# Kernel tuning notes

Measured on AMD Instinct MI355X. Metric: run time of the kernel, lower is better.

Reference implementation:

```python
import jax, jax.numpy as jnp
import numpy as np

N_NODES = 50000
N_EDGES = 800000
IN_DIM = 16
HID = 128
OUT_DIM = 1
N_LAYERS = 2


def setup_inputs() -> dict:
    key = jax.random.key(0)
    ks = jax.random.split(key, 16)
    s = 0.05
    inp = {
        "edge_feats": jax.random.normal(ks[0], (N_EDGES, IN_DIM), jnp.float32),
        "node_feats": jax.random.normal(ks[1], (N_NODES, 4), jnp.float32),
        "src": jax.random.randint(ks[2], (N_EDGES,), 0, N_NODES, jnp.int32),
        "dst": jax.random.randint(ks[3], (N_EDGES,), 0, N_NODES, jnp.int32),
        # edge_embedding (dead in original forward, kept for faithfulness)
        "W_eemb": jax.random.normal(ks[4], (IN_DIM, HID), jnp.float32) * s,
        "b_eemb": jnp.zeros((HID,), jnp.float32),
        # node_embedding: Linear(4, hidden)
        "W_nemb": jax.random.normal(ks[5], (4, HID), jnp.float32) * s,
        "b_nemb": jnp.zeros((HID,), jnp.float32),
        # stacked GraphConv weights [n_layers, H, H]
        "gnn_W": jax.random.normal(ks[6], (N_LAYERS, HID, HID), jnp.float32) * s,
        "gnn_b": jnp.zeros((N_LAYERS, HID), jnp.float32),
        # output MLP
        "out_W1": jax.random.normal(ks[7], (HID, HID), jnp.float32) * s,
        "out_b1": jnp.zeros((HID,), jnp.float32),
        "out_W2": jax.random.normal(ks[8], (HID, OUT_DIM), jnp.float32) * s,
        "out_b2": jnp.zeros((OUT_DIM,), jnp.float32),
    }
    return inp


def reference(edge_feats, node_feats, src, dst, W_eemb, b_eemb, W_nemb, b_nemb,
              gnn_W, gnn_b, out_W1, out_b1, out_W2, out_b2):
    ones = jnp.ones((src.shape[0],), jnp.float32)
    deg_out = jnp.clip(jax.ops.segment_sum(ones, src, num_segments=N_NODES), 1.0)
    deg_in = jnp.clip(jax.ops.segment_sum(ones, dst, num_segments=N_NODES), 1.0)
    norm_out = deg_out ** -0.5  # [N]
    norm_in = deg_in ** -0.5    # [N]

    # edge_embedding output is dead code in the original forward (overwritten)
    _h_e = edge_feats @ W_eemb + b_eemb

    h = node_feats @ W_nemb + b_nemb  # [N, H]
    for l in range(N_LAYERS):
        # DGL GraphConv norm='both': D_out^{-1/2} gather -> scatter-sum -> D_in^{-1/2} -> W, b
        hs = h * norm_out[:, None]
        agg = jax.ops.segment_sum(hs[src], dst, num_segments=N_NODES)  # [N, H]
        h = agg * norm_in[:, None]
        h = h @ gnn_W[l] + gnn_b[l]
        h = jax.nn.relu(h)

    edge_h = h[src] + h[dst]  # apply_edges UDF, [E, H]
    x = jax.nn.relu(edge_h @ out_W1 + out_b1)
    return x @ out_W2 + out_b2  # [E, OUT_DIM]
```

## Files before the change

kernel.cpp:

```cpp
#include <hip/hip_runtime.h>

#define N_NODES 50000
#define N_EDGES 800000
#define HID 128
#define NB 256
#define NPB 196
#define TP 136

typedef __attribute__((ext_vector_type(8))) short bf16x8;
typedef __attribute__((ext_vector_type(4))) float f32x4;

__device__ __forceinline__ unsigned pack2bf(float a, float b) {
  unsigned ua = __float_as_uint(a);
  ua += 0x7FFFu + ((ua >> 16) & 1u);
  unsigned ub = __float_as_uint(b);
  ub += 0x7FFFu + ((ub >> 16) & 1u);
  return (ua >> 16) | (ub & 0xFFFF0000u);
}
#define BFLO(u) __uint_as_float((u) << 16)
#define BFHI(u) __uint_as_float((u) & 0xFFFF0000u)

__device__ __forceinline__ float2 unpk(unsigned u) {
  return make_float2(BFLO(u), BFHI(u));
}
__device__ __forceinline__ float2 f2add(float2 a, float2 b) {
  return make_float2(a.x + b.x, a.y + b.y);
}
__device__ __forceinline__ float2 f2max0(float2 a) {
  return make_float2(fmaxf(a.x, 0.f), fmaxf(a.y, 0.f));
}
__device__ __forceinline__ float2 f2fma(float2 a, float2 b, float2 c) {
  return make_float2(fmaf(a.x, b.x, c.x), fmaf(a.y, b.y, c.y));
}


__global__ __launch_bounds__(256) void p1_hist_kernel(
    const int* __restrict__ src, const int* __restrict__ dst,
    int* __restrict__ bcnt_d, int* __restrict__ bcnt_s) {
  __shared__ int hd[NB], hs[NB];
  int t = threadIdx.x;
  hd[t] = 0; hs[t] = 0;
  __syncthreads();
  for (int e = blockIdx.x * 256 + t; e < N_EDGES; e += gridDim.x * 256) {
    atomicAdd(&hd[dst[e] / NPB], 1);
    atomicAdd(&hs[src[e] / NPB], 1);
  }
  __syncthreads();
  if (hd[t]) atomicAdd(&bcnt_d[t], hd[t]);
  if (hs[t]) atomicAdd(&bcnt_s[t], hs[t]);
}

__global__ void p2_scan_kernel(const int* __restrict__ bcnt_d, const int* __restrict__ bcnt_s,
                               int* __restrict__ bofs_d, int* __restrict__ bofs_s,
                               int* __restrict__ cur_d, int* __restrict__ cur_s) {
  __shared__ int s[NB];
  int t = threadIdx.x;
  int v = bcnt_d[t];
  s[t] = v;
  __syncthreads();
  for (int o = 1; o < NB; o <<= 1) {
    int x = (t >= o) ? s[t - o] : 0;
    __syncthreads();
    s[t] += x;
    __syncthreads();
  }
  int ofs = s[t] - v;
  bofs_d[t] = ofs; cur_d[t] = ofs;
  if (t == NB - 1) bofs_d[NB] = s[t];
  __syncthreads();
  v = bcnt_s[t];
  s[t] = v;
  __syncthreads();
  for (int o = 1; o < NB; o <<= 1) {
    int x = (t >= o) ? s[t - o] : 0;
    __syncthreads();
    s[t] += x;
    __syncthreads();
  }
  ofs = s[t] - v;
  bofs_s[t] = ofs; cur_s[t] = ofs;
  if (t == NB - 1) bofs_s[NB] = s[t];
}

__global__ __launch_bounds__(256) void p3_scatter_both_kernel(
    const int* __restrict__ src, const int* __restrict__ dst,
    int* __restrict__ cur_d, int* __restrict__ cur_s,
    int2* __restrict__ sdst, int* __restrict__ ssrc) {
  __shared__ int bcd[NB], bbd[NB], bcs[NB], bbs[NB];
  int t = threadIdx.x;
  int base = blockIdx.x * 2048;
  bcd[t] = 0; bcs[t] = 0;
  __syncthreads();
  int mybd[8], myrd[8], mys[8], myp[8], mybs[8], myrs[8];
#pragma unroll
  for (int u = 0; u < 8; ++u) {
    int e = base + u * 256 + t;
    mybd[u] = -1;
    if (e < N_EDGES) {
      int s = src[e], d = dst[e];
      int bd = d / NPB;
      mybd[u] = bd;
      myrd[u] = atomicAdd(&bcd[bd], 1);
      mys[u] = s;
      myp[u] = ((d - bd * NPB) << 20) | e;
      int bs = s / NPB;
      mybs[u] = bs;
      myrs[u] = atomicAdd(&bcs[bs], 1);
    }
  }
  __syncthreads();
  {
    int cd = bcd[t];
    if (cd) bbd[t] = atomicAdd(&cur_d[t], cd);
    int cs = bcs[t];
    if (cs) bbs[t] = atomicAdd(&cur_s[t], cs);
  }
  __syncthreads();
#pragma unroll
  for (int u = 0; u < 8; ++u) {
    if (mybd[u] >= 0) {
      sdst[bbd[mybd[u]] + myrd[u]] = make_int2(mys[u], myp[u]);
      ssrc[bbs[mybs[u]] + myrs[u]] = mys[u];
    }
  }
}

__global__ __launch_bounds__(256) void p4_csr_kernel(
    const int2* __restrict__ sdst, const int* __restrict__ bofs_d,
    int* __restrict__ row_ofs, float* __restrict__ norm_in,
    int* __restrict__ csr_src, int* __restrict__ csr_eid) {
  __shared__ int hc[NB], sc[NB], cur[NB];
  int b = blockIdx.x, t = threadIdx.x;
  int base = bofs_d[b], cnt = bofs_d[b + 1] - base;
  hc[t] = 0;
  __syncthreads();
  for (int i = t; i < cnt; i += 256) atomicAdd(&hc[sdst[base + i].y >> 20], 1);
  __syncthreads();
  int v = hc[t];
  sc[t] = v;
  __syncthreads();
  for (int o = 1; o < NB; o <<= 1) {
    int x = (t >= o) ? sc[t - o] : 0;
    __syncthreads();
    sc[t] += x;
    __syncthreads();
  }
  int ofs = sc[t] - v;
  int node = b * NPB + t;
  if (t < NPB && node < N_NODES) {
    row_ofs[node] = base + ofs;
    norm_in[node] = rsqrtf((float)(v < 1 ? 1 : v));
  }
  cur[t] = base + ofs;
  if (b == 0 && t == 0) row_ofs[N_NODES] = N_EDGES;
  __syncthreads();
  for (int i = t; i < cnt; i += 256) {
    int2 e = sdst[base + i];
    int pos = atomicAdd(&cur[e.y >> 20], 1);
    csr_src[pos] = e.x;
    csr_eid[pos] = e.y & 0xFFFFF;
  }
}

__global__ __launch_bounds__(256) void p5_degout_kernel(
    const int* __restrict__ ssrc, const int* __restrict__ bofs_s,
    float* __restrict__ norm_out) {
  __shared__ int hc[NB];
  int b = blockIdx.x, t = threadIdx.x;
  int base = bofs_s[b], cnt = bofs_s[b + 1] - base;
  int lo = b * NPB;
  hc[t] = 0;
  __syncthreads();
  for (int i = t; i < cnt; i += 256) atomicAdd(&hc[ssrc[base + i] - lo], 1);
  __syncthreads();
  int node = lo + t;
  if (t < NPB && node < N_NODES) {
    int v = hc[t];
    norm_out[node] = rsqrtf((float)(v < 1 ? 1 : v));
  }
}

__global__ __launch_bounds__(256) void prep_w_kernel(
    const float* __restrict__ Wa, const float* __restrict__ Wb,
    const float* __restrict__ Wc, short* __restrict__ Wta,
    short* __restrict__ Wtb, short* __restrict__ Wtc) {
  int t = blockIdx.x * 256 + threadIdx.x;
  if (t < HID * HID) {
    int k = t >> 7, n = t & 127;
    Wta[n * HID + k] = (short)(pack2bf(Wa[t], 0.f) & 0xFFFFu);
    Wtb[n * HID + k] = (short)(pack2bf(Wb[t], 0.f) & 0xFFFFu);
    Wtc[n * HID + k] = (short)(pack2bf(Wc[t], 0.f) & 0xFFFFu);
  }
}


__global__ __launch_bounds__(256) void agg4_kernel(
    const float4* __restrict__ nf4, const float* __restrict__ no_,
    const int* __restrict__ csr_src, const int* __restrict__ row_ofs,
    float4* __restrict__ agg4, float* __restrict__ sno) {
  int wid = (blockIdx.x * blockDim.x + threadIdx.x) >> 6;
  int lane = threadIdx.x & 63;
  int g = lane >> 4, l = lane & 15;
  int v = wid * 4 + g;
  if (v >= N_NODES) return;
  int beg = row_ofs[v], end = row_ofs[v + 1];
  float ax = 0.f, ay = 0.f, az = 0.f, aw = 0.f, sn = 0.f;
  for (int i = beg + l; i < end; i += 16) {
    int s = csr_src[i];
    float w = no_[s];
    float4 n = nf4[s];
    ax += n.x * w; ay += n.y * w; az += n.z * w; aw += n.w * w;
    sn += w;
  }
#pragma unroll
  for (int o = 1; o < 16; o <<= 1) {
    ax += __shfl_xor(ax, o, 16);
    ay += __shfl_xor(ay, o, 16);
    az += __shfl_xor(az, o, 16);
    aw += __shfl_xor(aw, o, 16);
    sn += __shfl_xor(sn, o, 16);
  }
  if (l == 0) {
    agg4[v] = make_float4(ax, ay, az, aw);
    sno[v] = sn;
  }
}

__global__ __launch_bounds__(256) void gemm_l1_mfma(
    const float4* __restrict__ agg4, const float* __restrict__ sno,
    const float* __restrict__ ni_, const float* __restrict__ no_,
    const float* __restrict__ Wn, const float* __restrict__ bn,
    const short* __restrict__ Wt0, const float* __restrict__ b0,
    short* __restrict__ h1b, int nrows) {
  int t = threadIdx.x;
  int w = t >> 6, lane = t & 63;
  int m16 = lane & 15, quad = lane >> 4;
  int v0 = blockIdx.x * 64;
  int row = v0 + w * 16 + m16;
  bool rvalid = row < nrows;
  int rc = rvalid ? row : (nrows - 1);
  float4 a = agg4[rc];
  float sn = sno[rc], nin = ni_[rc];

  bf16x8 xfr[4];
#pragma unroll
  for (int kc = 0; kc < 4; ++kc) {
    union { unsigned u[4]; bf16x8 v; } cv;
#pragma unroll
    for (int jj = 0; jj < 4; ++jj) {
      int k0 = kc * 32 + quad * 8 + jj * 2;
      float x0 = (a.x * Wn[k0] + a.y * Wn[HID + k0] + a.z * Wn[2 * HID + k0] +
                  a.w * Wn[3 * HID + k0] + bn[k0] * sn) * nin;
      int k1 = k0 + 1;
      float x1 = (a.x * Wn[k1] + a.y * Wn[HID + k1] + a.z * Wn[2 * HID + k1] +
                  a.w * Wn[3 * HID + k1] + bn[k1] * sn) * nin;
      cv.u[jj] = pack2bf(x0, x1);
    }
    xfr[kc] = cv.v;
  }
  f32x4 acc[8];
#pragma unroll
  for (int nt = 0; nt < 8; ++nt) {
    acc[nt][0] = 0.f; acc[nt][1] = 0.f; acc[nt][2] = 0.f; acc[nt][3] = 0.f;
  }
#pragma unroll
  for (int nt = 0; nt < 8; ++nt) {
    const bf16x8* Wr = (const bf16x8*)(Wt0 + (size_t)(nt * 16 + m16) * HID);
#pragma unroll
    for (int kc = 0; kc < 4; ++kc)
      acc[nt] = __builtin_amdgcn_mfma_f32_16x16x32_bf16(Wr[kc * 4 + quad], xfr[kc],
                                                        acc[nt], 0, 0, 0);
  }
  if (rvalid) {
    float nov = no_[row];
#pragma unroll
    for (int nt = 0; nt < 8; ++nt) {
      int nb = nt * 16 + quad * 4;
      float4 bv = *(const float4*)&b0[nb];
      float r0 = fmaxf(acc[nt][0] + bv.x, 0.f) * nov;
      float r1 = fmaxf(acc[nt][1] + bv.y, 0.f) * nov;
      float r2 = fmaxf(acc[nt][2] + bv.z, 0.f) * nov;
      float r3 = fmaxf(acc[nt][3] + bv.w, 0.f) * nov;
      uint2 pk;
      pk.x = pack2bf(r0, r1);
      pk.y = pack2bf(r2, r3);
      *(uint2*)(h1b + (size_t)row * HID + nb) = pk;
    }
  }
}

__global__ __launch_bounds__(256) void aggregate_kernel(
    const uint4* __restrict__ hb, const int* __restrict__ row_ofs,
    const int* __restrict__ csr_src, const float* __restrict__ ni_,
    uint4* __restrict__ Ab) {
  int v = (blockIdx.x * blockDim.x + threadIdx.x) >> 6;
  int lane = threadIdx.x & 63;
  if (v >= N_NODES) return;
  int beg = row_ofs[v], end = row_ofs[v + 1];
  int g = lane >> 4, l = lane & 15;
  float2 acc2[4];
#pragma unroll
  for (int j = 0; j < 4; ++j) acc2[j] = make_float2(0.f, 0.f);
  for (int i = beg; i < end; i += 16) {
    int ss[4];
#pragma unroll
    for (int u = 0; u < 4; ++u) {
      int ii = i + 4 * u + g;
      ss[u] = (ii < end) ? csr_src[ii] : N_NODES;
    }
    uint4 X[4];
#pragma unroll
    for (int u = 0; u < 4; ++u) X[u] = hb[(size_t)ss[u] * 16 + l];
#pragma unroll
    for (int u = 0; u < 4; ++u) {
      acc2[0] = f2add(acc2[0], unpk(X[u].x));
      acc2[1] = f2add(acc2[1], unpk(X[u].y));
      acc2[2] = f2add(acc2[2], unpk(X[u].z));
      acc2[3] = f2add(acc2[3], unpk(X[u].w));
    }
  }
#pragma unroll
  for (int j = 0; j < 4; ++j) {
    acc2[j].x += __shfl_xor(acc2[j].x, 16, 64);
    acc2[j].x += __shfl_xor(acc2[j].x, 32, 64);
    acc2[j].y += __shfl_xor(acc2[j].y, 16, 64);
    acc2[j].y += __shfl_xor(acc2[j].y, 32, 64);
  }
  if (g == 0) {
    float n = ni_[v];
    uint4 pk;
    pk.x = pack2bf(acc2[0].x * n, acc2[0].y * n);
    pk.y = pack2bf(acc2[1].x * n, acc2[1].y * n);
    pk.z = pack2bf(acc2[2].x * n, acc2[2].y * n);
    pk.w = pack2bf(acc2[3].x * n, acc2[3].y * n);
    Ab[(size_t)v * 16 + l] = pk;
  }
}

__global__ __launch_bounds__(256) void gemm_dual_mfma(
    const short* __restrict__ Ab, const short* __restrict__ Wt0,
    const float* __restrict__ b0, const short* __restrict__ Wt1,
    short* __restrict__ yb, int nrows) {
  __shared__ short T1s[4][16 * TP];
  int t = threadIdx.x;
  int w = t >> 6, lane = t & 63;
  int m16 = lane & 15, quad = lane >> 4;
  int v0 = blockIdx.x * 64;
  int row = v0 + w * 16 + m16;
  bool rvalid = row < nrows;
  int rc = rvalid ? row : (nrows - 1);

  bf16x8 xfr[4];
  {
    const bf16x8* Ar = (const bf16x8*)(Ab + (size_t)rc * HID);
#pragma unroll
    for (int kc = 0; kc < 4; ++kc) xfr[kc] = Ar[kc * 4 + quad];
  }
  f32x4 acc[8];
#pragma unroll
  for (int nt = 0; nt < 8; ++nt) {
    acc[nt][0] = 0.f; acc[nt][1] = 0.f; acc[nt][2] = 0.f; acc[nt][3] = 0.f;
  }
#pragma unroll
  for (int nt = 0; nt < 8; ++nt) {
    const bf16x8* Wr = (const bf16x8*)(Wt0 + (size_t)(nt * 16 + m16) * HID);
#pragma unroll
    for (int kc = 0; kc < 4; ++kc)
      acc[nt] = __builtin_amdgcn_mfma_f32_16x16x32_bf16(Wr[kc * 4 + quad], xfr[kc],
                                                        acc[nt], 0, 0, 0);
  }
  short* T1w = &T1s[w][0];
#pragma unroll
  for (int nt = 0; nt < 8; ++nt) {
    int nb = nt * 16 + quad * 4;
    float4 bv = *(const float4*)&b0[nb];
    float r0 = fmaxf(acc[nt][0] + bv.x, 0.f);
    float r1 = fmaxf(acc[nt][1] + bv.y, 0.f);
    float r2 = fmaxf(acc[nt][2] + bv.z, 0.f);
    float r3 = fmaxf(acc[nt][3] + bv.w, 0.f);
    uint2 pk;
    pk.x = pack2bf(r0, r1);
    pk.y = pack2bf(r2, r3);
    *(uint2*)&T1w[m16 * TP + nb] = pk;
    acc[nt][0] = 0.f; acc[nt][1] = 0.f; acc[nt][2] = 0.f; acc[nt][3] = 0.f;
  }
  __syncthreads();
  bf16x8 tfr[4];
#pragma unroll
  for (int kc = 0; kc < 4; ++kc)
    tfr[kc] = *(const bf16x8*)&T1w[m16 * TP + kc * 32 + quad * 8];
#pragma unroll
  for (int nt = 0; nt < 8; ++nt) {
    const bf16x8* Wr = (const bf16x8*)(Wt1 + (size_t)(nt * 16 + m16) * HID);
#pragma unroll
    for (int kc = 0; kc < 4; ++kc)
      acc[nt] = __builtin_amdgcn_mfma_f32_16x16x32_bf16(Wr[kc * 4 + quad], tfr[kc],
                                                        acc[nt], 0, 0, 0);
  }
  if (rvalid) {
#pragma unroll
    for (int nt = 0; nt < 8; ++nt) {
      int nb = nt * 16 + quad * 4;
      uint2 pk;
      pk.x = pack2bf(acc[nt][0], acc[nt][1]);
      pk.y = pack2bf(acc[nt][2], acc[nt][3]);
      *(uint2*)(yb + (size_t)row * HID + nb) = pk;
    }
  }
}

__global__ __launch_bounds__(256) void edge_out_kernel(
    const int* __restrict__ csr_src, const int* __restrict__ csr_eid,
    const int* __restrict__ row_ofs, const uint4* __restrict__ yb,
    const float* __restrict__ b1, const float* __restrict__ w2,
    const float* __restrict__ b2, float* __restrict__ out) {
  int v = (blockIdx.x * blockDim.x + threadIdx.x) >> 6;
  int lane = threadIdx.x & 63;
  if (v >= N_NODES) return;
  int beg = row_ofs[v], end = row_ofs[v + 1];
  if (beg >= end) return;
  int g = lane >> 4, l = lane & 15;
  const float2* b12 = (const float2*)b1;
  const float2* w22 = (const float2*)w2;
  uint4 D = yb[(size_t)v * 16 + l];
  float2 d0 = f2add(unpk(D.x), b12[l * 4 + 0]);
  float2 d1 = f2add(unpk(D.y), b12[l * 4 + 1]);
  float2 d2 = f2add(unpk(D.z), b12[l * 4 + 2]);
  float2 d3 = f2add(unpk(D.w), b12[l * 4 + 3]);
  float2 w0 = w22[l * 4 + 0], w1 = w22[l * 4 + 1];
  float2 w2v = w22[l * 4 + 2], w3 = w22[l * 4 + 3];
  float ob2 = b2[0];
  for (int i = beg; i < end; i += 16) {
    int ii[4]; bool qq[4]; int ss[4];
#pragma unroll
    for (int u = 0; u < 4; ++u) {
      ii[u] = i + 4 * u + g;
      qq[u] = ii[u] < end;
      ss[u] = csr_src[qq[u] ? ii[u] : beg];
    }
    uint4 A[4];
#pragma unroll
    for (int u = 0; u < 4; ++u) A[u] = yb[(size_t)ss[u] * 16 + l];
#pragma unroll
    for (int u = 0; u < 4; ++u) {
      float2 p2;
      p2.x = 0.f; p2.y = 0.f;
      p2 = f2fma(f2max0(f2add(unpk(A[u].x), d0)), w0, p2);
      p2 = f2fma(f2max0(f2add(unpk(A[u].y), d1)), w1, p2);
      p2 = f2fma(f2max0(f2add(unpk(A[u].z), d2)), w2v, p2);
      p2 = f2fma(f2max0(f2add(unpk(A[u].w), d3)), w3, p2);
      float p = p2.x + p2.y;
      p += __shfl_down(p, 8, 16);
      p += __shfl_down(p, 4, 16);
      p += __shfl_down(p, 2, 16);
      p += __shfl_down(p, 1, 16);
      if (l == 0 && qq[u]) out[csr_eid[ii[u]]] = p + ob2;
    }
  }
}

extern "C" void kernel_launch(void* const* d_in, const int* in_sizes, int n_in,
                              void* d_out, int out_size, void* d_ws, size_t ws_size,
                              hipStream_t stream) {
  const float* node_feats = (const float*)d_in[1];
  const int*   src        = (const int*)d_in[2];
  const int*   dst        = (const int*)d_in[3];
  const float* W_nemb     = (const float*)d_in[6];
  const float* b_nemb     = (const float*)d_in[7];
  const float* gnn_W      = (const float*)d_in[8];
  const float* gnn_b      = (const float*)d_in[9];
  const float* out_W1     = (const float*)d_in[10];
  const float* out_b1     = (const float*)d_in[11];
  const float* out_W2     = (const float*)d_in[12];
  const float* out_b2     = (const float*)d_in[13];
  float* out = (float*)d_out;

  size_t off = 0;
  char* base = (char*)d_ws;
  auto alloc = [&](size_t nbytes) -> char* {
    off = (off + 255) & ~(size_t)255;
    char* p = base + off;
    off += nbytes;
    return p;
  };
  int*    bcnt2    = (int*)alloc(2 * NB * 4);
  int*    bofs_d   = (int*)alloc((NB + 1) * 4);
  int*    bofs_s   = (int*)alloc((NB + 1) * 4);
  int*    cur_d    = (int*)alloc(NB * 4);
  int*    cur_s    = (int*)alloc(NB * 4);
  float*  norm_out = (float*)alloc(N_NODES * 4);
  float*  norm_in  = (float*)alloc(N_NODES * 4);
  int*    row_ofs  = (int*)alloc((N_NODES + 1) * 4);
  int*    csr_src  = (int*)alloc((size_t)N_EDGES * 4);
  int*    csr_eid  = (int*)alloc((size_t)N_EDGES * 4);
  float4* agg4     = (float4*)alloc((size_t)N_NODES * 16);
  float*  sno      = (float*)alloc(N_NODES * 4);
  short*  Wta      = (short*)alloc((size_t)HID * HID * 2);
  short*  Wtb      = (short*)alloc((size_t)HID * HID * 2);
  short*  Wtc     = (short*)alloc((size_t)HID * HID * 2);
  short*  h1b      = (short*)alloc((size_t)(N_NODES + 1) * HID * 2);
  short*  Ab       = (short*)alloc((size_t)N_NODES * HID * 2);
  short*  ybs      = (short*)alloc((size_t)N_NODES * HID * 2);
  int2*   sdst     = (int2*)Ab;
  int*    ssrc     = (int*)ybs;
  int*    bcnt_d   = bcnt2;
  int*    bcnt_s   = bcnt2 + NB;
  (void)ws_size; (void)n_in; (void)in_sizes; (void)out_size;

  hipMemsetAsync(bcnt2, 0, 2 * NB * 4, stream);
  hipMemsetAsync(h1b + (size_t)N_NODES * HID, 0, HID * 2, stream);
  prep_w_kernel<<<(HID * HID + 255) / 256, 256, 0, stream>>>(
      gnn_W, gnn_W + (size_t)HID * HID, out_W1, Wta, Wtb, Wtc);
  p1_hist_kernel<<<128, 256, 0, stream>>>(src, dst, bcnt_d, bcnt_s);
  p2_scan_kernel<<<1, 256, 0, stream>>>(bcnt_d, bcnt_s, bofs_d, bofs_s, cur_d, cur_s);
  p3_scatter_both_kernel<<<(N_EDGES + 2047) / 2048, 256, 0, stream>>>(
      src, dst, cur_d, cur_s, sdst, ssrc);
  p4_csr_kernel<<<NB, 256, 0, stream>>>(sdst, bofs_d, row_ofs, norm_in, csr_src, csr_eid);
  p5_degout_kernel<<<NB, 256, 0, stream>>>(ssrc, bofs_s, norm_out);

  agg4_kernel<<<(N_NODES * 16 + 255) / 256, 256, 0, stream>>>(
      (const float4*)node_feats, norm_out, csr_src, row_ofs, agg4, sno);
  gemm_l1_mfma<<<(N_NODES + 63) / 64, 256, 0, stream>>>(
      agg4, sno, norm_in, norm_out, W_nemb, b_nemb, Wta, gnn_b, h1b, N_NODES);

  aggregate_kernel<<<(N_NODES * 64 + 255) / 256, 256, 0, stream>>>(
      (const uint4*)h1b, row_ofs, csr_src, norm_in, (uint4*)Ab);

  gemm_dual_mfma<<<(N_NODES + 63) / 64, 256, 0, stream>>>(
      Ab, Wtb, gnn_b + HID, Wtc, ybs, N_NODES);

  edge_out_kernel<<<(N_NODES * 64 + 255) / 256, 256, 0, stream>>>(
      csr_src, csr_eid, row_ofs, (const uint4*)ybs, out_b1, out_W2, out_b2, out);
}
```

Measured before the change: 309.5 us.

## Switch to fp16 storage and MFMA, fuse prep kernels, rewrite edge output per-edge

Replaces bf16 with fp16 throughout: fp16 MFMA, packed conversions via cvt_pkrtz, and the edge dot product done with packed half adds and fdot2. The weight-prep work is folded into the scan kernel and the degree-out pass into the CSR kernel, which cuts the number of launches. The edge output kernel now uses one thread per edge with a new csr_dst array, and half of out_b1 is folded into each node's y so the edge sum carries the full bias. In exchange fp16 has less range than bf16, each thread loads 512 bytes per edge with no reuse across lanes, and the extra csr_dst array costs memory traffic.

```diff
diff --git a/kernel.cpp b/kernel.cpp
--- a/kernel.cpp
+++ b/kernel.cpp
@@ -7,30 +7,44 @@
 #define NPB 196
 #define TP 136
 
-typedef __attribute__((ext_vector_type(8))) short bf16x8;
+typedef __attribute__((ext_vector_type(8))) _Float16 f16x8;
+typedef __attribute__((ext_vector_type(2))) _Float16 h2v;
+typedef __attribute__((ext_vector_type(2))) __fp16 fp16v2;
 typedef __attribute__((ext_vector_type(4))) float f32x4;
-
-__device__ __forceinline__ unsigned pack2bf(float a, float b) {
-  unsigned ua = __float_as_uint(a);
-  ua += 0x7FFFu + ((ua >> 16) & 1u);
-  unsigned ub = __float_as_uint(b);
-  ub += 0x7FFFu + ((ub >> 16) & 1u);
-  return (ua >> 16) | (ub & 0xFFFF0000u);
-}
-#define BFLO(u) __uint_as_float((u) << 16)
-#define BFHI(u) __uint_as_float((u) & 0xFFFF0000u)
-
-__device__ __forceinline__ float2 unpk(unsigned u) {
-  return make_float2(BFLO(u), BFHI(u));
-}
-__device__ __forceinline__ float2 f2add(float2 a, float2 b) {
-  return make_float2(a.x + b.x, a.y + b.y);
-}
-__device__ __forceinline__ float2 f2max0(float2 a) {
-  return make_float2(fmaxf(a.x, 0.f), fmaxf(a.y, 0.f));
-}
-__device__ __forceinline__ float2 f2fma(float2 a, float2 b, float2 c) {
-  return make_float2(fmaf(a.x, b.x, c.x), fmaf(a.y, b.y, c.y));
+typedef __attribute__((ext_vector_type(2))) float f32x2;
+
+__device__ __forceinline__ unsigned pkh(float a, float b) {
+  union { fp16v2 h; unsigned u; } c;
+  c.h = __builtin_amdgcn_cvt_pkrtz(a, b);
+  return c.u;
+}
+__device__ __forceinline__ h2v u2h(unsigned u) {
+  union { unsigned u; h2v h; } c;
+  c.u = u;
+  return c.h;
+}
+__device__ __forceinline__ f32x2 unpkh(unsigned u) {
+  h2v h = u2h(u);
+  f32x2 r;
+  r[0] = (float)h[0];
+  r[1] = (float)h[1];
+  return r;
+}
+__device__ __forceinline__ short f2hs(float f) {
+  union { _Float16 h; short s; } c;
+  c.h = (_Float16)f;
+  return c.s;
+}
+__device__ __forceinline__ float edot(unsigned a, unsigned b, unsigned w, float acc) {
+  h2v r = u2h(a) + u2h(b);
+  h2v z = {(_Float16)0.f, (_Float16)0.f};
+  r = __builtin_elementwise_max(r, z);
+#if __has_builtin(__builtin_amdgcn_fdot2)
+  return __builtin_amdgcn_fdot2(r, u2h(w), acc, false);
+#else
+  h2v wv = u2h(w);
+  return acc + (float)r[0] * (float)wv[0] + (float)r[1] * (float)wv[1];
+#endif
 }
 
 
@@ -50,9 +64,33 @@
   if (hs[t]) atomicAdd(&bcnt_s[t], hs[t]);
 }
 
-__global__ void p2_scan_kernel(const int* __restrict__ bcnt_d, const int* __restrict__ bcnt_s,
-                               int* __restrict__ bofs_d, int* __restrict__ bofs_s,
-                               int* __restrict__ cur_d, int* __restrict__ cur_s) {
+__global__ void p2_scan_prep_kernel(
+    const int* __restrict__ bcnt_d, const int* __restrict__ bcnt_s,
+    int* __restrict__ bofs_d, int* __restrict__ bofs_s,
+    int* __restrict__ cur_d, int* __restrict__ cur_s,
+    const float* __restrict__ Wa, const float* __restrict__ Wb,
+    const float* __restrict__ Wc, const float* __restrict__ w2f,
+    short* __restrict__ Wta, short* __restrict__ Wtb, short* __restrict__ Wtc,
+    unsigned* __restrict__ w2h, short* __restrict__ h1bz) {
+  int b = blockIdx.x;
+  if (b > 0) {
+    int t = (b - 1) * 256 + threadIdx.x;
+    if (t < HID * HID) {
+      int k = t >> 7, n = t & 127;
+      Wta[n * HID + k] = f2hs(Wa[t]);
+      Wtb[n * HID + k] = f2hs(Wb[t]);
+      Wtc[n * HID + k] = f2hs(Wc[t]);
+    }
+    if (b == 1) {
+      int t0 = threadIdx.x;
+      if (t0 < 64) {
+        w2h[t0] = pkh(w2f[2 * t0], w2f[2 * t0 + 1]);
+      } else if (t0 < 128) {
+        ((unsigned*)h1bz)[t0 - 64] = 0u;
+      }
+    }
+    return;
+  }
   __shared__ int s[NB];
   int t = threadIdx.x;
   int v = bcnt_d[t];
@@ -125,12 +163,30 @@
   }
 }
 
-__global__ __launch_bounds__(256) void p4_csr_kernel(
+__global__ __launch_bounds__(256) void p45_kernel(
     const int2* __restrict__ sdst, const int* __restrict__ bofs_d,
     int* __restrict__ row_ofs, float* __restrict__ norm_in,
-    int* __restrict__ csr_src, int* __restrict__ csr_eid) {
+    int* __restrict__ csr_src, int* __restrict__ csr_eid, int* __restrict__ csr_dst,
+    const int* __restrict__ ssrc, const int* __restrict__ bofs_s,
+    float* __restrict__ norm_out) {
   __shared__ int hc[NB], sc[NB], cur[NB];
-  int b = blockIdx.x, t = threadIdx.x;
+  int t = threadIdx.x;
+  if (blockIdx.x >= NB) {
+    int b = blockIdx.x - NB;
+    int base = bofs_s[b], cnt = bofs_s[b + 1] - base;
+    int lo = b * NPB;
+    hc[t] = 0;
+    __syncthreads();
+    for (int i = t; i < cnt; i += 256) atomicAdd(&hc[ssrc[base + i] - lo], 1);
+    __syncthreads();
+    int node = lo + t;
+    if (t < NPB && node < N_NODES) {
+      int v = hc[t];
+      norm_out[node] = rsqrtf((float)(v < 1 ? 1 : v));
+    }
+    return;
+  }
+  int b = blockIdx.x;
   int base = bofs_d[b], cnt = bofs_d[b + 1] - base;
   hc[t] = 0;
   __syncthreads();
@@ -156,40 +212,11 @@
   __syncthreads();
   for (int i = t; i < cnt; i += 256) {
     int2 e = sdst[base + i];
-    int pos = atomicAdd(&cur[e.y >> 20], 1);
+    int loc = e.y >> 20;
+    int pos = atomicAdd(&cur[loc], 1);
     csr_src[pos] = e.x;
     csr_eid[pos] = e.y & 0xFFFFF;
-  }
-}
-
-__global__ __launch_bounds__(256) void p5_degout_kernel(
-    const int* __restrict__ ssrc, const int* __restrict__ bofs_s,
-    float* __restrict__ norm_out) {
-  __shared__ int hc[NB];
-  int b = blockIdx.x, t = threadIdx.x;
-  int base = bofs_s[b], cnt = bofs_s[b + 1] - base;
-  int lo = b * NPB;
-  hc[t] = 0;
-  __syncthreads();
-  for (int i = t; i < cnt; i += 256) atomicAdd(&hc[ssrc[base + i] - lo], 1);
-  __syncthreads();
-  int node = lo + t;
-  if (t < NPB && node < N_NODES) {
-    int v = hc[t];
-    norm_out[node] = rsqrtf((float)(v < 1 ? 1 : v));
-  }
-}
-
-__global__ __launch_bounds__(256) void prep_w_kernel(
-    const float* __restrict__ Wa, const float* __restrict__ Wb,
-    const float* __restrict__ Wc, short* __restrict__ Wta,
-    short* __restrict__ Wtb, short* __restrict__ Wtc) {
-  int t = blockIdx.x * 256 + threadIdx.x;
-  if (t < HID * HID) {
-    int k = t >> 7, n = t & 127;
-    Wta[n * HID + k] = (short)(pack2bf(Wa[t], 0.f) & 0xFFFFu);
-    Wtb[n * HID + k] = (short)(pack2bf(Wb[t], 0.f) & 0xFFFFu);
-    Wtc[n * HID + k] = (short)(pack2bf(Wc[t], 0.f) & 0xFFFFu);
+    csr_dst[pos] = b * NPB + loc;
   }
 }
 
@@ -242,10 +269,10 @@
   float4 a = agg4[rc];
   float sn = sno[rc], nin = ni_[rc];
 
-  bf16x8 xfr[4];
+  f16x8 xfr[4];
 #pragma unroll
   for (int kc = 0; kc < 4; ++kc) {
-    union { unsigned u[4]; bf16x8 v; } cv;
+    union { unsigned u[4]; f16x8 v; } cv;
 #pragma unroll
     for (int jj = 0; jj < 4; ++jj) {
       int k0 = kc * 32 + quad * 8 + jj * 2;
@@ -254,7 +281,7 @@
       int k1 = k0 + 1;
       float x1 = (a.x * Wn[k1] + a.y * Wn[HID + k1] + a.z * Wn[2 * HID + k1] +
                   a.w * Wn[3 * HID + k1] + bn[k1] * sn) * nin;
-      cv.u[jj] = pack2bf(x0, x1);
+      cv.u[jj] = pkh(x0, x1);
     }
     xfr[kc] = cv.v;
   }
@@ -265,11 +292,11 @@
   }
 #pragma unroll
   for (int nt = 0; nt < 8; ++nt) {
-    const bf16x8* Wr = (const bf16x8*)(Wt0 + (size_t)(nt * 16 + m16) * HID);
+    const f16x8* Wr = (const f16x8*)(Wt0 + (size_t)(nt * 16 + m16) * HID);
 #pragma unroll
     for (int kc = 0; kc < 4; ++kc)
-      acc[nt] = __builtin_amdgcn_mfma_f32_16x16x32_bf16(Wr[kc * 4 + quad], xfr[kc],
-                                                        acc[nt], 0, 0, 0);
+      acc[nt] = __builtin_amdgcn_mfma_f32_16x16x32_f16(Wr[kc * 4 + quad], xfr[kc],
+                                                       acc[nt], 0, 0, 0);
   }
   if (rvalid) {
     float nov = no_[row];
@@ -282,8 +309,8 @@
       float r2 = fmaxf(acc[nt][2] + bv.z, 0.f) * nov;
       float r3 = fmaxf(acc[nt][3] + bv.w, 0.f) * nov;
       uint2 pk;
-      pk.x = pack2bf(r0, r1);
-      pk.y = pack2bf(r2, r3);
+      pk.x = pkh(r0, r1);
+      pk.y = pkh(r2, r3);
       *(uint2*)(h1b + (size_t)row * HID + nb) = pk;
     }
   }
@@ -298,9 +325,9 @@
   if (v >= N_NODES) return;
   int beg = row_ofs[v], end = row_ofs[v + 1];
   int g = lane >> 4, l = lane & 15;
-  float2 acc2[4];
-#pragma unroll
-  for (int j = 0; j < 4; ++j) acc2[j] = make_float2(0.f, 0.f);
+  f32x2 acc2[4];
+#pragma unroll
+  for (int j = 0; j < 4; ++j) acc2[j] = (f32x2){0.f, 0.f};
   for (int i = beg; i < end; i += 16) {
     int ss[4];
 #pragma unroll
@@ -313,26 +340,26 @@
     for (int u = 0; u < 4; ++u) X[u] = hb[(size_t)ss[u] * 16 + l];
 #pragma unroll
     for (int u = 0; u < 4; ++u) {
-      acc2[0] = f2add(acc2[0], unpk(X[u].x));
-      acc2[1] = f2add(acc2[1], unpk(X[u].y));
-      acc2[2] = f2add(acc2[2], unpk(X[u].z));
-      acc2[3] = f2add(acc2[3], unpk(X[u].w));
+      acc2[0] += unpkh(X[u].x);
+      acc2[1] += unpkh(X[u].y);
+      acc2[2] += unpkh(X[u].z);
+      acc2[3] += unpkh(X[u].w);
     }
   }
 #pragma unroll
   for (int j = 0; j < 4; ++j) {
-    acc2[j].x += __shfl_xor(acc2[j].x, 16, 64);
-    acc2[j].x += __shfl_xor(acc2[j].x, 32, 64);
-    acc2[j].y += __shfl_xor(acc2[j].y, 16, 64);
-    acc2[j].y += __shfl_xor(acc2[j].y, 32, 64);
+    acc2[j][0] += __shfl_xor(acc2[j][0], 16, 64);
+    acc2[j][0] += __shfl_xor(acc2[j][0], 32, 64);
+    acc2[j][1] += __shfl_xor(acc2[j][1], 16, 64);
+    acc2[j][1] += __shfl_xor(acc2[j][1], 32, 64);
   }
   if (g == 0) {
     float n = ni_[v];
     uint4 pk;
-    pk.x = pack2bf(acc2[0].x * n, acc2[0].y * n);
-    pk.y = pack2bf(acc2[1].x * n, acc2[1].y * n);
-    pk.z = pack2bf(acc2[2].x * n, acc2[2].y * n);
-    pk.w = pack2bf(acc2[3].x * n, acc2[3].y * n);
+    pk.x = pkh(acc2[0][0] * n, acc2[0][1] * n);
+    pk.y = pkh(acc2[1][0] * n, acc2[1][1] * n);
+    pk.z = pkh(acc2[2][0] * n, acc2[2][1] * n);
+    pk.w = pkh(acc2[3][0] * n, acc2[3][1] * n);
     Ab[(size_t)v * 16 + l] = pk;
   }
 }
@@ -340,7 +367,7 @@
 __global__ __launch_bounds__(256) void gemm_dual_mfma(
     const short* __restrict__ Ab, const short* __restrict__ Wt0,
     const float* __restrict__ b0, const short* __restrict__ Wt1,
-    short* __restrict__ yb, int nrows) {
+    const float* __restrict__ b1o, short* __restrict__ yb, int nrows) {
   __shared__ short T1s[4][16 * TP];
   int t = threadIdx.x;
   int w = t >> 6, lane = t & 63;
@@ -350,9 +377,9 @@
   bool rvalid = row < nrows;
   int rc = rvalid ? row : (nrows - 1);
 
-  bf16x8 xfr[4];
+  f16x8 xfr[4];
   {
-    const bf16x8* Ar = (const bf16x8*)(Ab + (size_t)rc * HID);
+    const f16x8* Ar = (const f16x8*)(Ab + (size_t)rc * HID);
 #pragma unroll
     for (int kc = 0; kc < 4; ++kc) xfr[kc] = Ar[kc * 4 + quad];
   }
@@ -363,11 +390,11 @@
   }
 #pragma unroll
   for (int nt = 0; nt < 8; ++nt) {
-    const bf16x8* Wr = (const bf16x8*)(Wt0 + (size_t)(nt * 16 + m16) * HID);
+    const f16x8* Wr = (const f16x8*)(Wt0 + (size_t)(nt * 16 + m16) * HID);
 #pragma unroll
     for (int kc = 0; kc < 4; ++kc)
-      acc[nt] = __builtin_amdgcn_mfma_f32_16x16x32_bf16(Wr[kc * 4 + quad], xfr[kc],
-                                                        acc[nt], 0, 0, 0);
+      acc[nt] = __builtin_amdgcn_mfma_f32_16x16x32_f16(Wr[kc * 4 + quad], xfr[kc],
+                                                       acc[nt], 0, 0, 0);
   }
   short* T1w = &T1s[w][0];
 #pragma unroll
@@ -379,84 +406,68 @@
     float r2 = fmaxf(acc[nt][2] + bv.z, 0.f);
     float r3 = fmaxf(acc[nt][3] + bv.w, 0.f);
     uint2 pk;
-    pk.x = pack2bf(r0, r1);
-    pk.y = pack2bf(r2, r3);
+    pk.x = pkh(r0, r1);
+    pk.y = pkh(r2, r3);
     *(uint2*)&T1w[m16 * TP + nb] = pk;
     acc[nt][0] = 0.f; acc[nt][1] = 0.f; acc[nt][2] = 0.f; acc[nt][3] = 0.f;
   }
   __syncthreads();
-  bf16x8 tfr[4];
+  f16x8 tfr[4];
 #pragma unroll
   for (int kc = 0; kc < 4; ++kc)
-    tfr[kc] = *(const bf16x8*)&T1w[m16 * TP + kc * 32 + quad * 8];
+    tfr[kc] = *(const f16x8*)&T1w[m16 * TP + kc * 32 + quad * 8];
 #pragma unroll
   for (int nt = 0; nt < 8; ++nt) {
-    const bf16x8* Wr = (const bf16x8*)(Wt1 + (size_t)(nt * 16 + m16) * HID);
+    const f16x8* Wr = (const f16x8*)(Wt1 + (size_t)(nt * 16 + m16) * HID);
 #pragma unroll
     for (int kc = 0; kc < 4; ++kc)
-      acc[nt] = __builtin_amdgcn_mfma_f32_16x16x32_bf16(Wr[kc * 4 + quad], tfr[kc],
-                                                        acc[nt], 0, 0, 0);
+      acc[nt] = __builtin_amdgcn_mfma_f32_16x16x32_f16(Wr[kc * 4 + quad], tfr[kc],
+                                                       acc[nt], 0, 0, 0);
   }
   if (rvalid) {
 #pragma unroll
     for (int nt = 0; nt < 8; ++nt) {
       int nb = nt * 16 + quad * 4;
+      float4 bv = *(const float4*)&b1o[nb];
       uint2 pk;
-      pk.x = pack2bf(acc[nt][0], acc[nt][1]);
-      pk.y = pack2bf(acc[nt][2], acc[nt][3]);
+      pk.x = pkh(acc[nt][0] + 0.5f * bv.x, acc[nt][1] + 0.5f * bv.y);
+      pk.y = pkh(acc[nt][2] + 0.5f * bv.z, acc[nt][3] + 0.5f * bv.w);
       *(uint2*)(yb + (size_t)row * HID + nb) = pk;
     }
   }
 }
 
 __global__ __launch_bounds__(256) void edge_out_kernel(
-    const int* __restrict__ csr_src, const int* __restrict__ csr_eid,
-    const int* __restrict__ row_ofs, const uint4* __restrict__ yb,
-    const float* __restrict__ b1, const float* __restrict__ w2,
-    const float* __restrict__ b2, float* __restrict__ out) {
-  int v = (blockIdx.x * blockDim.x + threadIdx.x) >> 6;
-  int lane = threadIdx.x & 63;
-  if (v >= N_NODES) return;
-  int beg = row_ofs[v], end = row_ofs[v + 1];
-  if (beg >= end) return;
-  int g = lane >> 4, l = lane & 15;
-  const float2* b12 = (const float2*)b1;
-  const float2* w22 = (const float2*)w2;
-  uint4 D = yb[(size_t)v * 16 + l];
-  float2 d0 = f2add(unpk(D.x), b12[l * 4 + 0]);
-  float2 d1 = f2add(unpk(D.y), b12[l * 4 + 1]);
-  float2 d2 = f2add(unpk(D.z), b12[l * 4 + 2]);
-  float2 d3 = f2add(unpk(D.w), b12[l * 4 + 3]);
-  float2 w0 = w22[l * 4 + 0], w1 = w22[l * 4 + 1];
-  float2 w2v = w22[l * 4 + 2], w3 = w22[l * 4 + 3];
+    const int* __restrict__ csr_src, const int* __restrict__ csr_dst,
+    const int* __restrict__ csr_eid, const uint4* __restrict__ yb,
+    const unsigned* __restrict__ w2h, const float* __restrict__ b2,
+    float* __restrict__ out) {
+  int i = blockIdx.x * 256 + threadIdx.x;
+  if (i >= N_EDGES) return;
+  int s = csr_src[i];
+  int d = csr_dst[i];
+  int eid = csr_eid[i];
   float ob2 = b2[0];
-  for (int i = beg; i < end; i += 16) {
-    int ii[4]; bool qq[4]; int ss[4];
-#pragma unroll
-    for (int u = 0; u < 4; ++u) {
-      ii[u] = i + 4 * u + g;
-      qq[u] = ii[u] < end;
-      ss[u] = csr_src[qq[u] ? ii[u] : beg];
-    }
-    uint4 A[4];
-#pragma unroll
-    for (int u = 0; u < 4; ++u) A[u] = yb[(size_t)ss[u] * 16 + l];
-#pragma unroll
-    for (int u = 0; u < 4; ++u) {
-      float2 p2;
-      p2.x = 0.f; p2.y = 0.f;
-      p2 = f2fma(f2max0(f2add(unpk(A[u].x), d0)), w0, p2);
-      p2 = f2fma(f2max0(f2add(unpk(A[u].y), d1)), w1, p2);
-      p2 = f2fma(f2max0(f2add(unpk(A[u].z), d2)), w2v, p2);
-      p2 = f2fma(f2max0(f2add(unpk(A[u].w), d3)), w3, p2);
-      float p = p2.x + p2.y;
-      p += __shfl_down(p, 8, 16);
-      p += __shfl_down(p, 4, 16);
-      p += __shfl_down(p, 2, 16);
-      p += __shfl_down(p, 1, 16);
-      if (l == 0 && qq[u]) out[csr_eid[ii[u]]] = p + ob2;
-    }
-  }
+  const uint4* ys = yb + (size_t)s * 16;
+  const uint4* yd = yb + (size_t)d * 16;
+  float p0 = 0.f, p1 = 0.f;
+#pragma unroll
+  for (int h = 0; h < 2; ++h) {
+    uint4 A[8], B[8];
+#pragma unroll
+    for (int c = 0; c < 8; ++c) A[c] = ys[h * 8 + c];
+#pragma unroll
+    for (int c = 0; c < 8; ++c) B[c] = yd[h * 8 + c];
+#pragma unroll
+    for (int c = 0; c < 8; ++c) {
+      int wb = h * 32 + c * 4;
+      p0 = edot(A[c].x, B[c].x, w2h[wb + 0], p0);
+      p1 = edot(A[c].y, B[c].y, w2h[wb + 1], p1);
+      p0 = edot(A[c].z, B[c].z, w2h[wb + 2], p0);
+      p1 = edot(A[c].w, B[c].w, w2h[wb + 3], p1);
+    }
+  }
+  out[eid] = p0 + p1 + ob2;
 }
 
 extern "C" void kernel_launch(void* const* d_in, const int* in_sizes, int n_in,
@@ -493,11 +504,13 @@
   int*    row_ofs  = (int*)alloc((N_NODES + 1) * 4);
   int*    csr_src  = (int*)alloc((size_t)N_EDGES * 4);
   int*    csr_eid  = (int*)alloc((size_t)N_EDGES * 4);
+  int*    csr_dst  = (int*)alloc((size_t)N_EDGES * 4);
   float4* agg4     = (float4*)alloc((size_t)N_NODES * 16);
   float*  sno      = (float*)alloc(N_NODES * 4);
   short*  Wta      = (short*)alloc((size_t)HID * HID * 2);
   short*  Wtb      = (short*)alloc((size_t)HID * HID * 2);
-  short*  Wtc     = (short*)alloc((size_t)HID * HID * 2);
+  short*  Wtc      = (short*)alloc((size_t)HID * HID * 2);
+  unsigned* w2h    = (unsigned*)alloc(64 * 4);
   short*  h1b      = (short*)alloc((size_t)(N_NODES + 1) * HID * 2);
   short*  Ab       = (short*)alloc((size_t)N_NODES * HID * 2);
   short*  ybs      = (short*)alloc((size_t)N_NODES * HID * 2);
@@ -507,16 +520,17 @@
   int*    bcnt_s   = bcnt2 + NB;
   (void)ws_size; (void)n_in; (void)in_sizes; (void)out_size;
 
-  hipMemsetAsync(bcnt2, 0, 2 * NB * 4, stream);
-  hipMemsetAsync(h1b + (size_t)N_NODES * HID, 0, HID * 2, stream);
-  prep_w_kernel<<<(HID * HID + 255) / 256, 256, 0, stream>>>(
-      gnn_W, gnn_W + (size_t)HID * HID, out_W1, Wta, Wtb, Wtc);
+  (void)hipMemsetAsync(bcnt2, 0, 2 * NB * 4, stream);
   p1_hist_kernel<<<128, 256, 0, stream>>>(src, dst, bcnt_d, bcnt_s);
-  p2_scan_kernel<<<1, 256, 0, stream>>>(bcnt_d, bcnt_s, bofs_d, bofs_s, cur_d, cur_s);
+  p2_scan_prep_kernel<<<65, 256, 0, stream>>>(
+      bcnt_d, bcnt_s, bofs_d, bofs_s, cur_d, cur_s,
+      gnn_W, gnn_W + (size_t)HID * HID, out_W1, out_W2,
+      Wta, Wtb, Wtc, w2h, h1b + (size_t)N_NODES * HID);
   p3_scatter_both_kernel<<<(N_EDGES + 2047) / 2048, 256, 0, stream>>>(
       src, dst, cur_d, cur_s, sdst, ssrc);
-  p4_csr_kernel<<<NB, 256, 0, stream>>>(sdst, bofs_d, row_ofs, norm_in, csr_src, csr_eid);
-  p5_degout_kernel<<<NB, 256, 0, stream>>>(ssrc, bofs_s, norm_out);
+  p45_kernel<<<2 * NB, 256, 0, stream>>>(
+      sdst, bofs_d, row_ofs, norm_in, csr_src, csr_eid, csr_dst,
+      ssrc, bofs_s, norm_out);
 
   agg4_kernel<<<(N_NODES * 16 + 255) / 256, 256, 0, stream>>>(
       (const float4*)node_feats, norm_out, csr_src, row_ofs, agg4, sno);
@@ -527,8 +541,8 @@
       (const uint4*)h1b, row_ofs, csr_src, norm_in, (uint4*)Ab);
 
   gemm_dual_mfma<<<(N_NODES + 63) / 64, 256, 0, stream>>>(
-      Ab, Wtb, gnn_b + HID, Wtc, ybs, N_NODES);
-
-  edge_out_kernel<<<(N_NODES * 64 + 255) / 256, 256, 0, stream>>>(
-      csr_src, csr_eid, row_ofs, (const uint4*)ybs, out_b1, out_W2, out_b2, out);
-}
+      Ab, Wtb, gnn_b + HID, Wtc, out_b1, ybs, N_NODES);
+
+  edge_out_kernel<<<(N_EDGES + 255) / 256, 256, 0, stream>>>(
+      csr_src, csr_dst, csr_eid, (const uint4*)ybs, w2h, out_b2, out);
+}
```

New measurement: 312.1 us. No clear change (+0.8%).
